# Kernel optimization log

Hardware: AMD Instinct MI355X
Metric: run time of the kernel (lower is better)

Reference implementation:

```python
import jax, jax.numpy as jnp
import numpy as np

B = 16384
F = 1024
DELTA = 0.3
LAMB = 0.0005


def setup_inputs() -> dict:
    key = jax.random.key(0)
    k1, k2, k3, k4 = jax.random.split(key, 4)
    skt = jax.random.normal(k1, (B, F), dtype=jnp.float32)
    imgp = jax.random.normal(k2, (B, F), dtype=jnp.float32)
    imgn = jax.random.normal(k3, (B, F), dtype=jnp.float32)
    eye = jnp.eye(F, dtype=jnp.float32)
    w = eye + 0.05 * jax.random.normal(k4, (F, F), dtype=jnp.float32)
    return {"skt": skt, "imgp": imgp, "imgn": imgn, "w": w, "eye": eye}


def _distance(v1, v2, w, w_rowsum, w_colsum):
    # sum_{i,j} w[i,j] * (v1[:,i] - v2[:,j])**2
    #   = (v1**2) @ w.sum(1) - 2 * v1 @ w @ v2^T (diag) + (v2**2) @ w.sum(0)
    cross = ((v1 @ w) * v2).sum(axis=-1)  # [B]
    return (v1 * v1) @ w_rowsum - 2.0 * cross + (v2 * v2) @ w_colsum


def reference(skt, imgp, imgn, w, eye):
    w_rowsum = w.sum(axis=1)  # [F]
    w_colsum = w.sum(axis=0)  # [F]
    dp = _distance(skt, imgp, w, w_rowsum, w_colsum)  # [B]
    dn = _distance(skt, imgn, w, w_rowsum, w_colsum)  # [B]
    hinge = jnp.maximum(DELTA + dp - dn, 0.0).mean()
    dw = w - eye
    regu = jnp.abs(dw).sum() + jnp.sqrt((dw * dw).sum())
    return hinge + LAMB * regu
```

## Files before the change

kernel.cpp:

```cpp
#include <hip/hip_runtime.h>
#include <hip/hip_bf16.h>

#define FDIM 1024
#define BROWS 16384
#define DELTA_C 0.3f
#define LAMB_C 0.0005f

typedef __bf16 bf8v __attribute__((ext_vector_type(8)));
typedef float f4v __attribute__((ext_vector_type(4)));
typedef unsigned short u16;
typedef u16 u16x8 __attribute__((ext_vector_type(8)));

#define WS_PABS_OFF 4160
#define WS_PSQ_OFF 4672
#define WS_ROWACC_OFF 8192
#define WS_WB_OFF 131072
#define WS_SKTB_OFF (131072 + (1u << 21))
#define WS_NEED_FULL ((size_t)WS_SKTB_OFF + ((size_t)1 << 25))

__device__ __forceinline__ u16 f2bf(float f) {
  unsigned u = __builtin_bit_cast(unsigned, f);
  u += 0x7fffu + ((u >> 16) & 1u);
  return (u16)(u >> 16);
}

__device__ __forceinline__ void gload_lds16(const void* g, void* l) {
  __builtin_amdgcn_global_load_lds(
      (const __attribute__((address_space(1))) unsigned int*)g,
      (__attribute__((address_space(3))) unsigned int*)l, 16, 0, 0);
}

template <bool DO_A>
__global__ __launch_bounds__(256) void prep_all(const float* __restrict__ w,
                                                const float* __restrict__ skt,
                                                float* __restrict__ colsum,
                                                float* __restrict__ pabs,
                                                float* __restrict__ psq,
                                                u16* __restrict__ wb,
                                                u16* __restrict__ sktb) {
  __shared__ char smem_u[17440];
  const int t = threadIdx.x;
  const int bid = blockIdx.x;

  if (bid < 128) {
    u16(*tile)[1024] = (u16(*)[1024])smem_u;
    float* red = (float*)(smem_u + 16384);
    const int b = bid;
    const int k0 = b * 8;
    const int col = t * 4;

    float cs0 = 0.f, cs1 = 0.f, cs2 = 0.f, cs3 = 0.f;
    float aacc = 0.f, sacc = 0.f;
#pragma unroll
    for (int i = 0; i < 8; ++i) {
      const int gk = k0 + i;
      const float4 v = *(const float4*)(w + (size_t)gk * FDIM + col);
      ushort4 bb;
      bb.x = f2bf(v.x); bb.y = f2bf(v.y); bb.z = f2bf(v.z); bb.w = f2bf(v.w);
      *(ushort4*)(&tile[i][col]) = bb;
      cs0 += v.x; cs1 += v.y; cs2 += v.z; cs3 += v.w;
      const float d0 = v.x - (gk == col + 0 ? 1.f : 0.f);
      const float d1 = v.y - (gk == col + 1 ? 1.f : 0.f);
      const float d2 = v.z - (gk == col + 2 ? 1.f : 0.f);
      const float d3 = v.w - (gk == col + 3 ? 1.f : 0.f);
      aacc += fabsf(d0) + fabsf(d1) + fabsf(d2) + fabsf(d3);
      sacc += d0 * d0 + d1 * d1 + d2 * d2 + d3 * d3;
    }
    atomicAdd(&colsum[col + 0], cs0);
    atomicAdd(&colsum[col + 1], cs1);
    atomicAdd(&colsum[col + 2], cs2);
    atomicAdd(&colsum[col + 3], cs3);
#pragma unroll
    for (int off = 1; off < 64; off <<= 1) {
      aacc += __shfl_xor(aacc, off);
      sacc += __shfl_xor(sacc, off);
    }
    const int wid = t >> 6;
    if ((t & 63) == 0) { red[wid] = aacc; red[4 + wid] = sacc; }
    __syncthreads();
    if (t == 0) pabs[b] = red[0] + red[1] + red[2] + red[3];
    if (t == 1) psq[b] = red[4] + red[5] + red[6] + red[7];
#pragma unroll
    for (int j = 0; j < 4; ++j) {
      const int n = col + j;
      u16x8 pk;
#pragma unroll
      for (int e = 0; e < 8; ++e) pk[e] = tile[e][n];
      *(u16x8*)(wb + ((size_t)b * FDIM + n) * 8) = pk;
    }
  } else if constexpr (DO_A) {
    u16(*tile)[136] = (u16(*)[136])smem_u;
    const int ab = bid - 128;
    const int mb = ab >> 3;
    const int kb = ab & 7;
    const int m0 = mb * 64, k0 = kb * 128;
#pragma unroll
    for (int i = 0; i < 8; ++i) {
      const int fid = i * 256 + t;
      const int ml = fid >> 5;
      const int c4 = fid & 31;
      const float4 v = *(const float4*)(skt + (size_t)(m0 + ml) * FDIM + k0 + c4 * 4);
      ushort4 b;
      b.x = f2bf(v.x); b.y = f2bf(v.y); b.z = f2bf(v.z); b.w = f2bf(v.w);
      *(ushort4*)(&tile[ml][c4 * 4]) = b;
    }
    __syncthreads();
    const int ks0 = k0 >> 3;
#pragma unroll
    for (int i = 0; i < 4; ++i) {
      const int uid = i * 256 + t;
      const int si = uid >> 6;
      const int ml = uid & 63;
      const u16x8 pk = *(const u16x8*)(&tile[ml][si * 8]);
      *(u16x8*)(sktb + ((size_t)(ks0 + si) * BROWS + m0 + ml) * 8) = pk;
    }
  }
}

template <bool PRE>
__global__ __launch_bounds__(256, 3) void hofel_main(
    const float* __restrict__ skt, const float* __restrict__ imgp,
    const float* __restrict__ imgn, const u16* __restrict__ wb,
    const u16* __restrict__ sktb, const float* __restrict__ colsum,
    float* __restrict__ rowacc) {
  __shared__ u16 ldsT[16384];
  __shared__ float lds_cs[128];

  const int t = threadIdx.x;
  const int lane = t & 63;
  const int wid = t >> 6;
  const int l15 = lane & 15;
  const int l4 = lane >> 4;

  const int swz = (blockIdx.x & 7) * 128 + (blockIdx.x >> 3);
  const int mt = swz >> 3, nt = swz & 7;
  const int m0 = mt * 128, n0 = nt * 128;

  if (t < 128) lds_cs[t] = colsum[n0 + t];

  const int wm = (wid >> 1) * 64;
  const int wn = (wid & 1) * 64;

  f4v acc[4][4];
#pragma unroll
  for (int mi = 0; mi < 4; ++mi)
#pragma unroll
    for (int ni = 0; ni < 4; ++ni) {
      f4v z = {0.f, 0.f, 0.f, 0.f};
      acc[mi][ni] = z;
    }

  for (int kt = 0; kt < 16; ++kt) {
    __syncthreads();
    if constexpr (PRE) {
#pragma unroll
      for (int r = 0; r < 8; ++r) {
        const int o = r * 4096 + wid * 1024;
        const int ol = o + lane * 16;
        const char* src;
        if (ol < 16384) {
          const int s = ol >> 11;
          const int m = (ol >> 4) & 127;
          src = (const char*)(sktb + ((size_t)(kt * 8 + s) * BROWS + m0 + m) * 8);
        } else {
          const int o2 = ol - 16384;
          const int s = o2 >> 11;
          const int n = (o2 >> 4) & 127;
          src = (const char*)(wb + ((size_t)(kt * 8 + s) * FDIM + n0 + n) * 8);
        }
        gload_lds16(src, (char*)ldsT + o);
      }
    } else {
#pragma unroll
      for (int r = 0; r < 4; ++r) {
        const int o = r * 4096 + wid * 1024;
        const int ol = o + lane * 16;
        const int s = ol >> 11;
        const int n = (ol >> 4) & 127;
        gload_lds16((const char*)(wb + ((size_t)(kt * 8 + s) * FDIM + n0 + n) * 8),
                    (char*)ldsT + 16384 + o);
      }
      const int m = t >> 1, h = t & 1;
      const float* ap = skt + (size_t)(m0 + m) * FDIM + kt * 64 + h * 32;
#pragma unroll
      for (int q = 0; q < 4; ++q) {
        const float4 v0 = *(const float4*)(ap + q * 8);
        const float4 v1 = *(const float4*)(ap + q * 8 + 4);
        u16x8 pk;
        pk[0] = f2bf(v0.x); pk[1] = f2bf(v0.y); pk[2] = f2bf(v0.z); pk[3] = f2bf(v0.w);
        pk[4] = f2bf(v1.x); pk[5] = f2bf(v1.y); pk[6] = f2bf(v1.z); pk[7] = f2bf(v1.w);
        *(u16x8*)((char*)ldsT + ((h * 4 + q) * 128 + m) * 16) = pk;
      }
    }
    __syncthreads();

#pragma unroll
    for (int kk = 0; kk < 2; ++kk) {
      bf8v aF[4], bF[4];
#pragma unroll
      for (int mi = 0; mi < 4; ++mi)
        aF[mi] = *(const bf8v*)((char*)ldsT + (((kk * 4 + l4) * 128) + wm + mi * 16 + l15) * 16);
#pragma unroll
      for (int ni = 0; ni < 4; ++ni)
        bF[ni] = *(const bf8v*)((char*)ldsT + 16384 + (((kk * 4 + l4) * 128) + wn + ni * 16 + l15) * 16);
#pragma unroll
      for (int mi = 0; mi < 4; ++mi)
#pragma unroll
        for (int ni = 0; ni < 4; ++ni)
          acc[mi][ni] = __builtin_amdgcn_mfma_f32_16x16x32_bf16(aF[mi], bF[ni], acc[mi][ni], 0, 0, 0);
    }
  }

#pragma unroll
  for (int mi = 0; mi < 4; ++mi) {
#pragma unroll
    for (int rr = 0; rr < 4; ++rr) {
      const int row = m0 + wm + mi * 16 + l4 * 4 + rr;
      const float* pr = imgp + (size_t)row * FDIM + n0;
      const float* nr = imgn + (size_t)row * FDIM + n0;
      float s = 0.f;
#pragma unroll
      for (int ni = 0; ni < 4; ++ni) {
        const int cl = wn + ni * 16 + l15;
        const float T = acc[mi][ni][rr];
        const float p = pr[cl];
        const float q = nr[cl];
        s += (p - q) * (-2.f * T + (p + q) * lds_cs[cl]);
      }
#pragma unroll
      for (int off = 1; off < 16; off <<= 1) s += __shfl_xor(s, off);
      if (l15 == 0) atomicAdd(rowacc + row, s);
    }
  }
}

__global__ __launch_bounds__(1024) void hinge_reduce(const float* __restrict__ rowacc,
                                                     float* __restrict__ wsf) {
  __shared__ float part[16];
  const int t = threadIdx.x;
  const int id = blockIdx.x * 1024 + t;
  float v = fmaxf(DELTA_C + rowacc[id], 0.f);
#pragma unroll
  for (int off = 1; off < 64; off <<= 1) v += __shfl_xor(v, off);
  if ((t & 63) == 0) part[t >> 6] = v;
  __syncthreads();
  if (t < 16) {
    float x = part[t];
#pragma unroll
    for (int off = 1; off < 16; off <<= 1) x += __shfl_xor(x, off);
    if (t == 0) atomicAdd(&wsf[0], x);
  }
}

__global__ __launch_bounds__(128) void finalize_k(const float* __restrict__ wsf,
                                                  const float* __restrict__ pabs,
                                                  const float* __restrict__ psq,
                                                  float* __restrict__ out) {
  __shared__ float ra[2], rs[2];
  const int t = threadIdx.x;
  float a = pabs[t], s = psq[t];
#pragma unroll
  for (int off = 1; off < 64; off <<= 1) {
    a += __shfl_xor(a, off);
    s += __shfl_xor(s, off);
  }
  if ((t & 63) == 0) { ra[t >> 6] = a; rs[t >> 6] = s; }
  __syncthreads();
  if (t == 0)
    out[0] = wsf[0] * (1.f / (float)BROWS) +
             LAMB_C * ((ra[0] + ra[1]) + sqrtf(rs[0] + rs[1]));
}

extern "C" void kernel_launch(void* const* d_in, const int* in_sizes, int n_in,
                              void* d_out, int out_size, void* d_ws, size_t ws_size,
                              hipStream_t stream) {
  const float* skt  = (const float*)d_in[0];
  const float* imgp = (const float*)d_in[1];
  const float* imgn = (const float*)d_in[2];
  const float* w    = (const float*)d_in[3];

  float* wsf = (float*)d_ws;
  float* colsum = wsf + 16;
  float* pabs = (float*)((char*)d_ws + WS_PABS_OFF);
  float* psq = (float*)((char*)d_ws + WS_PSQ_OFF);
  float* rowacc = (float*)((char*)d_ws + WS_ROWACC_OFF);
  u16* wb = (u16*)((char*)d_ws + WS_WB_OFF);
  u16* sktb = (u16*)((char*)d_ws + WS_SKTB_OFF);
  float* out = (float*)d_out;

  hipMemsetAsync(d_ws, 0, WS_ROWACC_OFF + BROWS * sizeof(float), stream);

  if (ws_size >= WS_NEED_FULL) {
    prep_all<true><<<128 + 2048, 256, 0, stream>>>(w, skt, colsum, pabs, psq, wb, sktb);
    hofel_main<true><<<1024, 256, 0, stream>>>(skt, imgp, imgn, wb, sktb, colsum, rowacc);
  } else {
    prep_all<false><<<128, 256, 0, stream>>>(w, skt, colsum, pabs, psq, wb, sktb);
    hofel_main<false><<<1024, 256, 0, stream>>>(skt, imgp, imgn, wb, sktb, colsum, rowacc);
  }

  hinge_reduce<<<16, 1024, 0, stream>>>(rowacc, wsf);
  finalize_k<<<1, 128, 0, stream>>>(wsf, pabs, psq, out);
}
```

Measured before the change: 88.63 us.

## Double-buffer LDS and enlarge GEMM tile to 256x128 with 512 threads

The main kernel now computes a 256x128 output tile per block with 8 waves instead of 128x128 with 4 waves, which halves the grid. The K loop moves in steps of 32 through two LDS buffers, so the load of the next K slice is issued while the current slice is being multiplied. This removes one of the two barriers per step and reuses each weight tile across more rows. In exchange, each block uses more LDS and registers, which may lower the number of resident blocks per CU, and each step now does fewer MFMAs between barriers.

Result: no change. 87.64 us (-1.1%).

```diff
diff --git a/kernel.cpp b/kernel.cpp
--- a/kernel.cpp
+++ b/kernel.cpp
@@ -118,12 +118,12 @@
 }
 
 template <bool PRE>
-__global__ __launch_bounds__(256, 3) void hofel_main(
+__global__ __launch_bounds__(512, 4) void hofel_main(
     const float* __restrict__ skt, const float* __restrict__ imgp,
     const float* __restrict__ imgn, const u16* __restrict__ wb,
     const u16* __restrict__ sktb, const float* __restrict__ colsum,
     float* __restrict__ rowacc) {
-  __shared__ u16 ldsT[16384];
+  __shared__ u16 ldsT[2][12288];
   __shared__ float lds_cs[128];
 
   const int t = threadIdx.x;
@@ -132,14 +132,12 @@
   const int l15 = lane & 15;
   const int l4 = lane >> 4;
 
-  const int swz = (blockIdx.x & 7) * 128 + (blockIdx.x >> 3);
+  const int swz = (blockIdx.x & 7) * 64 + (blockIdx.x >> 3);
   const int mt = swz >> 3, nt = swz & 7;
-  const int m0 = mt * 128, n0 = nt * 128;
-
-  if (t < 128) lds_cs[t] = colsum[n0 + t];
-
-  const int wm = (wid >> 1) * 64;
-  const int wn = (wid & 1) * 64;
+  const int m0 = mt * 256, n0 = nt * 128;
+
+  const int wr = wid >> 1, wc = wid & 1;
+  const int wm = wr * 64, wn = wc * 64;
 
   f4v acc[4][4];
 #pragma unroll
@@ -150,65 +148,72 @@
       acc[mi][ni] = z;
     }
 
-  for (int kt = 0; kt < 16; ++kt) {
-    __syncthreads();
+  auto stage = [&](int buf, int kt) {
     if constexpr (PRE) {
 #pragma unroll
-      for (int r = 0; r < 8; ++r) {
-        const int o = r * 4096 + wid * 1024;
+      for (int r = 0; r < 3; ++r) {
+        const int o = r * 8192 + wid * 1024;
         const int ol = o + lane * 16;
         const char* src;
         if (ol < 16384) {
-          const int s = ol >> 11;
-          const int m = (ol >> 4) & 127;
-          src = (const char*)(sktb + ((size_t)(kt * 8 + s) * BROWS + m0 + m) * 8);
+          const int s = ol >> 12;
+          const int m = (ol >> 4) & 255;
+          src = (const char*)(sktb + ((size_t)(kt * 4 + s) * BROWS + m0 + m) * 8);
         } else {
           const int o2 = ol - 16384;
           const int s = o2 >> 11;
           const int n = (o2 >> 4) & 127;
-          src = (const char*)(wb + ((size_t)(kt * 8 + s) * FDIM + n0 + n) * 8);
+          src = (const char*)(wb + ((size_t)(kt * 4 + s) * FDIM + n0 + n) * 8);
         }
-        gload_lds16(src, (char*)ldsT + o);
+        gload_lds16(src, (char*)ldsT[buf] + o);
       }
     } else {
-#pragma unroll
-      for (int r = 0; r < 4; ++r) {
-        const int o = r * 4096 + wid * 1024;
+      {
+        const int o = wid * 1024;
         const int ol = o + lane * 16;
         const int s = ol >> 11;
         const int n = (ol >> 4) & 127;
-        gload_lds16((const char*)(wb + ((size_t)(kt * 8 + s) * FDIM + n0 + n) * 8),
-                    (char*)ldsT + 16384 + o);
+        gload_lds16((const char*)(wb + ((size_t)(kt * 4 + s) * FDIM + n0 + n) * 8),
+                    (char*)ldsT[buf] + 16384 + o);
       }
       const int m = t >> 1, h = t & 1;
-      const float* ap = skt + (size_t)(m0 + m) * FDIM + kt * 64 + h * 32;
-#pragma unroll
-      for (int q = 0; q < 4; ++q) {
+      const float* ap = skt + (size_t)(m0 + m) * FDIM + kt * 32 + h * 16;
+#pragma unroll
+      for (int q = 0; q < 2; ++q) {
         const float4 v0 = *(const float4*)(ap + q * 8);
         const float4 v1 = *(const float4*)(ap + q * 8 + 4);
         u16x8 pk;
         pk[0] = f2bf(v0.x); pk[1] = f2bf(v0.y); pk[2] = f2bf(v0.z); pk[3] = f2bf(v0.w);
         pk[4] = f2bf(v1.x); pk[5] = f2bf(v1.y); pk[6] = f2bf(v1.z); pk[7] = f2bf(v1.w);
-        *(u16x8*)((char*)ldsT + ((h * 4 + q) * 128 + m) * 16) = pk;
+        *(u16x8*)((char*)ldsT[buf] + (h * 2 + q) * 4096 + m * 16) = pk;
       }
     }
+  };
+
+  stage(0, 0);
+  if (t < 128) lds_cs[t] = colsum[n0 + t];
+  __syncthreads();
+
+  int cur = 0;
+  for (int kt = 0; kt < 32; ++kt) {
+    if (kt < 31) stage(cur ^ 1, kt + 1);
+
+    const char* bufb = (const char*)ldsT[cur];
+    bf8v aF[4], bF[4];
+#pragma unroll
+    for (int mi = 0; mi < 4; ++mi)
+      aF[mi] = *(const bf8v*)(bufb + l4 * 4096 + (wm + mi * 16 + l15) * 16);
+#pragma unroll
+    for (int ni = 0; ni < 4; ++ni)
+      bF[ni] = *(const bf8v*)(bufb + 16384 + l4 * 2048 + (wn + ni * 16 + l15) * 16);
+#pragma unroll
+    for (int mi = 0; mi < 4; ++mi)
+#pragma unroll
+      for (int ni = 0; ni < 4; ++ni)
+        acc[mi][ni] = __builtin_amdgcn_mfma_f32_16x16x32_bf16(aF[mi], bF[ni], acc[mi][ni], 0, 0, 0);
+
     __syncthreads();
-
-#pragma unroll
-    for (int kk = 0; kk < 2; ++kk) {
-      bf8v aF[4], bF[4];
-#pragma unroll
-      for (int mi = 0; mi < 4; ++mi)
-        aF[mi] = *(const bf8v*)((char*)ldsT + (((kk * 4 + l4) * 128) + wm + mi * 16 + l15) * 16);
-#pragma unroll
-      for (int ni = 0; ni < 4; ++ni)
-        bF[ni] = *(const bf8v*)((char*)ldsT + 16384 + (((kk * 4 + l4) * 128) + wn + ni * 16 + l15) * 16);
-#pragma unroll
-      for (int mi = 0; mi < 4; ++mi)
-#pragma unroll
-        for (int ni = 0; ni < 4; ++ni)
-          acc[mi][ni] = __builtin_amdgcn_mfma_f32_16x16x32_bf16(aF[mi], bF[ni], acc[mi][ni], 0, 0, 0);
-    }
+    cur ^= 1;
   }
 
 #pragma unroll
@@ -292,10 +297,10 @@
 
   if (ws_size >= WS_NEED_FULL) {
     prep_all<true><<<128 + 2048, 256, 0, stream>>>(w, skt, colsum, pabs, psq, wb, sktb);
-    hofel_main<true><<<1024, 256, 0, stream>>>(skt, imgp, imgn, wb, sktb, colsum, rowacc);
+    hofel_main<true><<<512, 512, 0, stream>>>(skt, imgp, imgn, wb, sktb, colsum, rowacc);
   } else {
     prep_all<false><<<128, 256, 0, stream>>>(w, skt, colsum, pabs, psq, wb, sktb);
-    hofel_main<false><<<1024, 256, 0, stream>>>(skt, imgp, imgn, wb, sktb, colsum, rowacc);
+    hofel_main<false><<<512, 512, 0, stream>>>(skt, imgp, imgn, wb, sktb, colsum, rowacc);
   }
 
   hinge_reduce<<<16, 1024, 0, stream>>>(rowacc, wsf);
```
